# Kernel optimization log

Measured on AMD Instinct MI355X. Metric: run time of the kernel, lower is better.

Reference implementation:

```python
import jax, jax.numpy as jnp
import numpy as np

POOL = 7  # pool_size


def _src_coords(start, size, P):
    """TF1 resize_images bilinear (align_corners=False): src = out_idx * in/out.
    start,size: (R,) int32 crop offset/extent. Returns abs low/high idx and frac, all (R,P)."""
    j = jnp.arange(P, dtype=jnp.float32)  # (P,)
    s = j[None, :] * (size[:, None].astype(jnp.float32) / P)  # (R,P) coords inside crop
    i0 = jnp.floor(s).astype(jnp.int32)
    i1 = jnp.minimum(i0 + 1, size[:, None] - 1)
    frac = s - i0.astype(jnp.float32)
    return start[:, None] + i0, start[:, None] + i1, frac


def roi_pool(img, rois, P):
    # img: (1,H,W,C) float; rois: (1,R,4) as (x,y,w,h) -> cast to int32 like the original
    im = img[0]  # (H,W,C)
    r = rois[0].astype(jnp.int32)  # (R,4)
    x, y, w, h = r[:, 0], r[:, 1], r[:, 2], r[:, 3]
    H, W = im.shape[0], im.shape[1]
    ax0, ax1, fx = _src_coords(x, w, P)  # (R,P)
    ay0, ay1, fy = _src_coords(y, h, P)  # (R,P)
    ax0 = jnp.clip(ax0, 0, W - 1); ax1 = jnp.clip(ax1, 0, W - 1)
    ay0 = jnp.clip(ay0, 0, H - 1); ay1 = jnp.clip(ay1, 0, H - 1)
    # broadcasted corner gathers -> (R,P,P,C)
    v00 = im[ay0[:, :, None], ax0[:, None, :]]
    v01 = im[ay0[:, :, None], ax1[:, None, :]]
    v10 = im[ay1[:, :, None], ax0[:, None, :]]
    v11 = im[ay1[:, :, None], ax1[:, None, :]]
    fx_ = fx[:, None, :, None]  # broadcast over y-dim and channels
    fy_ = fy[:, :, None, None]
    top = v00 * (1.0 - fx_) + v01 * fx_
    bot = v10 * (1.0 - fx_) + v11 * fx_
    out = top * (1.0 - fy_) + bot * fy_  # (R,P,P,C)
    return out[None]  # (1,R,P,P,C)


def setup_inputs() -> dict:
    key = jax.random.key(0)
    k1, k2, k3, k4, k5 = jax.random.split(key, 5)
    H = W = 100
    C = 1024
    R = 512
    img = jax.random.normal(k1, (1, H, W, C), dtype=jnp.float32)
    x = jax.random.randint(k2, (1, R), 0, 50)
    y = jax.random.randint(k3, (1, R), 0, 50)
    w = jax.random.randint(k4, (1, R), 1, 51)
    h = jax.random.randint(k5, (1, R), 1, 51)
    rois = jnp.stack([x, y, w, h], axis=-1).astype(jnp.float32)  # (1,R,4)
    return {"img": img, "rois": rois}


def reference(img, rois):
    return roi_pool(img, rois, POOL)
```

## Files before the change

kernel.cpp:

```cpp
#include <hip/hip_runtime.h>


#define IMG_H 100
#define IMG_W 100
#define IMG_C 1024
#define N_ROI 512
#define POOLP 7

__global__ __launch_bounds__(256) void roi_pool_kernel(
    const float* __restrict__ img,
    const float* __restrict__ rois,
    float* __restrict__ out)
{
    const int p   = blockIdx.x;
    const int roi = p / 49;
    const int pos = p - roi * 49;
    const int py  = pos / 7;
    const int px  = pos - py * 7;

    const float4 rv = *reinterpret_cast<const float4*>(rois + roi * 4);
    const int x = (int)rv.x;
    const int y = (int)rv.y;
    const int w = (int)rv.z;
    const int h = (int)rv.w;

    const float sx  = (float)px * ((float)w / (float)POOLP);
    const int   ix0 = (int)floorf(sx);
    const int   ix1 = min(ix0 + 1, w - 1);
    const float fx  = sx - (float)ix0;
    const int   ax0 = min(max(x + ix0, 0), IMG_W - 1);
    const int   ax1 = min(max(x + ix1, 0), IMG_W - 1);

    const float sy  = (float)py * ((float)h / (float)POOLP);
    const int   iy0 = (int)floorf(sy);
    const int   iy1 = min(iy0 + 1, h - 1);
    const float fy  = sy - (float)iy0;
    const int   ay0 = min(max(y + iy0, 0), IMG_H - 1);
    const int   ay1 = min(max(y + iy1, 0), IMG_H - 1);

    const float gx = 1.0f - fx;
    const float gy = 1.0f - fy;

    const int c = threadIdx.x << 2;

    const float4 v00 = *reinterpret_cast<const float4*>(
        img + ((size_t)ay0 * IMG_W + ax0) * IMG_C + c);
    const float4 v01 = *reinterpret_cast<const float4*>(
        img + ((size_t)ay0 * IMG_W + ax1) * IMG_C + c);
    const float4 v10 = *reinterpret_cast<const float4*>(
        img + ((size_t)ay1 * IMG_W + ax0) * IMG_C + c);
    const float4 v11 = *reinterpret_cast<const float4*>(
        img + ((size_t)ay1 * IMG_W + ax1) * IMG_C + c);

    float4 o;
    o.x = (v00.x * gx + v01.x * fx) * gy + (v10.x * gx + v11.x * fx) * fy;
    o.y = (v00.y * gx + v01.y * fx) * gy + (v10.y * gx + v11.y * fx) * fy;
    o.z = (v00.z * gx + v01.z * fx) * gy + (v10.z * gx + v11.z * fx) * fy;
    o.w = (v00.w * gx + v01.w * fx) * gy + (v10.w * gx + v11.w * fx) * fy;

    *reinterpret_cast<float4*>(out + (size_t)p * IMG_C + c) = o;
}

extern "C" void kernel_launch(void* const* d_in, const int* in_sizes, int n_in,
                              void* d_out, int out_size, void* d_ws, size_t ws_size,
                              hipStream_t stream)
{
    const float* img  = (const float*)d_in[0];
    const float* rois = (const float*)d_in[1];
    float* out = (float*)d_out;

    const int n_blocks = N_ROI * POOLP * POOLP;
    roi_pool_kernel<<<n_blocks, 256, 0, stream>>>(img, rois, out);
}
```

Measured before the change: 162.4 us.

## Use persistent blocks with software-pipelined gathers, XCD-aware block mapping, nontemporal stores

```diff
diff --git a/kernel.cpp b/kernel.cpp
--- a/kernel.cpp
+++ b/kernel.cpp
@@ -6,19 +6,23 @@
 #define IMG_C 1024
 #define N_ROI 512
 #define POOLP 7
+#define NPOS  (N_ROI * POOLP * POOLP)
+#define NBLK  2048
 
-__global__ __launch_bounds__(256) void roi_pool_kernel(
-    const float* __restrict__ img,
-    const float* __restrict__ rois,
-    float* __restrict__ out)
+typedef float f32x4 __attribute__((ext_vector_type(4)));
+
+__device__ __forceinline__ void pos_setup(
+    const float* __restrict__ img, const float* __restrict__ rois,
+    int p, int c,
+    const f32x4*& q00, const f32x4*& q01, const f32x4*& q10, const f32x4*& q11,
+    float& fx, float& fy)
 {
-    const int p   = blockIdx.x;
     const int roi = p / 49;
     const int pos = p - roi * 49;
     const int py  = pos / 7;
     const int px  = pos - py * 7;
 
-    const float4 rv = *reinterpret_cast<const float4*>(rois + roi * 4);
+    const f32x4 rv = *reinterpret_cast<const f32x4*>(rois + roi * 4);
     const int x = (int)rv.x;
     const int y = (int)rv.y;
     const int w = (int)rv.z;
@@ -27,38 +31,74 @@
     const float sx  = (float)px * ((float)w / (float)POOLP);
     const int   ix0 = (int)floorf(sx);
     const int   ix1 = min(ix0 + 1, w - 1);
-    const float fx  = sx - (float)ix0;
-    const int   ax0 = min(max(x + ix0, 0), IMG_W - 1);
-    const int   ax1 = min(max(x + ix1, 0), IMG_W - 1);
+    fx = sx - (float)ix0;
+    const int ax0 = min(max(x + ix0, 0), IMG_W - 1);
+    const int ax1 = min(max(x + ix1, 0), IMG_W - 1);
 
     const float sy  = (float)py * ((float)h / (float)POOLP);
     const int   iy0 = (int)floorf(sy);
     const int   iy1 = min(iy0 + 1, h - 1);
-    const float fy  = sy - (float)iy0;
-    const int   ay0 = min(max(y + iy0, 0), IMG_H - 1);
-    const int   ay1 = min(max(y + iy1, 0), IMG_H - 1);
+    fy = sy - (float)iy0;
+    const int ay0 = min(max(y + iy0, 0), IMG_H - 1);
+    const int ay1 = min(max(y + iy1, 0), IMG_H - 1);
 
+    q00 = reinterpret_cast<const f32x4*>(img + ((size_t)(ay0 * IMG_W + ax0) * IMG_C + c));
+    q01 = reinterpret_cast<const f32x4*>(img + ((size_t)(ay0 * IMG_W + ax1) * IMG_C + c));
+    q10 = reinterpret_cast<const f32x4*>(img + ((size_t)(ay1 * IMG_W + ax0) * IMG_C + c));
+    q11 = reinterpret_cast<const f32x4*>(img + ((size_t)(ay1 * IMG_W + ax1) * IMG_C + c));
+}
+
+__device__ __forceinline__ f32x4 blend(
+    f32x4 v00, f32x4 v01, f32x4 v10, f32x4 v11, float fx, float fy)
+{
     const float gx = 1.0f - fx;
     const float gy = 1.0f - fy;
+    f32x4 top = v00 * gx + v01 * fx;
+    f32x4 bot = v10 * gx + v11 * fx;
+    return top * gy + bot * fy;
+}
+
+__global__ __launch_bounds__(256) void roi_pool_kernel(
+    const float* __restrict__ img,
+    const float* __restrict__ rois,
+    float* __restrict__ out)
+{
+    const int b = blockIdx.x;
+    const int cid = ((b & 7) << 8) | (b >> 3);
+    const int p0  = (int)(((long long)cid       * NPOS) / NBLK);
+    const int p1  = (int)(((long long)(cid + 1) * NPOS) / NBLK);
+    if (p0 >= p1) return;
 
     const int c = threadIdx.x << 2;
 
-    const float4 v00 = *reinterpret_cast<const float4*>(
-        img + ((size_t)ay0 * IMG_W + ax0) * IMG_C + c);
-    const float4 v01 = *reinterpret_cast<const float4*>(
-        img + ((size_t)ay0 * IMG_W + ax1) * IMG_C + c);
-    const float4 v10 = *reinterpret_cast<const float4*>(
-        img + ((size_t)ay1 * IMG_W + ax0) * IMG_C + c);
-    const float4 v11 = *reinterpret_cast<const float4*>(
-        img + ((size_t)ay1 * IMG_W + ax1) * IMG_C + c);
+    const f32x4 *q00, *q01, *q10, *q11;
+    float fx, fy;
+    pos_setup(img, rois, p0, c, q00, q01, q10, q11, fx, fy);
+    f32x4 v00 = *q00;
+    f32x4 v01 = *q01;
+    f32x4 v10 = *q10;
+    f32x4 v11 = *q11;
 
-    float4 o;
-    o.x = (v00.x * gx + v01.x * fx) * gy + (v10.x * gx + v11.x * fx) * fy;
-    o.y = (v00.y * gx + v01.y * fx) * gy + (v10.y * gx + v11.y * fx) * fy;
-    o.z = (v00.z * gx + v01.z * fx) * gy + (v10.z * gx + v11.z * fx) * fy;
-    o.w = (v00.w * gx + v01.w * fx) * gy + (v10.w * gx + v11.w * fx) * fy;
+    for (int p = p0 + 1; p < p1; ++p) {
+        const f32x4 *r00, *r01, *r10, *r11;
+        float nfx, nfy;
+        pos_setup(img, rois, p, c, r00, r01, r10, r11, nfx, nfy);
+        f32x4 w00 = *r00;
+        f32x4 w01 = *r01;
+        f32x4 w10 = *r10;
+        f32x4 w11 = *r11;
 
-    *reinterpret_cast<float4*>(out + (size_t)p * IMG_C + c) = o;
+        const f32x4 o = blend(v00, v01, v10, v11, fx, fy);
+        __builtin_nontemporal_store(
+            o, reinterpret_cast<f32x4*>(out + (size_t)(p - 1) * IMG_C + c));
+
+        v00 = w00; v01 = w01; v10 = w10; v11 = w11;
+        fx = nfx; fy = nfy;
+    }
+
+    const f32x4 o = blend(v00, v01, v10, v11, fx, fy);
+    __builtin_nontemporal_store(
+        o, reinterpret_cast<f32x4*>(out + (size_t)(p1 - 1) * IMG_C + c));
 }
 
 extern "C" void kernel_launch(void* const* d_in, const int* in_sizes, int n_in,
@@ -69,6 +109,5 @@
     const float* rois = (const float*)d_in[1];
     float* out = (float*)d_out;
 
-    const int n_blocks = N_ROI * POOLP * POOLP;
-    roi_pool_kernel<<<n_blocks, 256, 0, stream>>>(img, rois, out);
+    roi_pool_kernel<<<NBLK, 256, 0, stream>>>(img, rois, out);
 }
```

After: 169.2 us. 1.04x slower.

## Persistent grid with XCD-aware ROI partitioning and nontemporal output stores

Applied to the files above, without the earlier changes.

```diff
diff --git a/kernel.cpp b/kernel.cpp
--- a/kernel.cpp
+++ b/kernel.cpp
@@ -6,59 +6,83 @@
 #define IMG_C 1024
 #define N_ROI 512
 #define POOLP 7
+#define NPOS  (N_ROI * POOLP * POOLP)
+#define NBLK  4096
+#define ROI_PER_XCD   (N_ROI / 8)
+#define UNITS_PER_XCD (ROI_PER_XCD * 49)
+#define BLK_PER_XCD   (NBLK / 8)
 
-__global__ __launch_bounds__(256) void roi_pool_kernel(
+typedef float f32x4 __attribute__((ext_vector_type(4)));
+
+__global__ __launch_bounds__(128) void roi_pool_kernel(
     const float* __restrict__ img,
     const float* __restrict__ rois,
     float* __restrict__ out)
 {
-    const int p   = blockIdx.x;
-    const int roi = p / 49;
-    const int pos = p - roi * 49;
-    const int py  = pos / 7;
-    const int px  = pos - py * 7;
+    const int b    = blockIdx.x;
+    const int xcd  = b & 7;
+    const int l    = b >> 3;
+    const int base = xcd * UNITS_PER_XCD;
 
-    const float4 rv = *reinterpret_cast<const float4*>(rois + roi * 4);
-    const int x = (int)rv.x;
-    const int y = (int)rv.y;
-    const int w = (int)rv.z;
-    const int h = (int)rv.w;
+    const int c0 = threadIdx.x << 2;
+    const int c1 = c0 + 512;
 
-    const float sx  = (float)px * ((float)w / (float)POOLP);
-    const int   ix0 = (int)floorf(sx);
-    const int   ix1 = min(ix0 + 1, w - 1);
-    const float fx  = sx - (float)ix0;
-    const int   ax0 = min(max(x + ix0, 0), IMG_W - 1);
-    const int   ax1 = min(max(x + ix1, 0), IMG_W - 1);
+    for (int u = l; u < UNITS_PER_XCD; u += BLK_PER_XCD) {
+        const int p   = base + u;
+        const int roi = p / 49;
+        const int pos = p - roi * 49;
+        const int py  = pos / 7;
+        const int px  = pos - py * 7;
 
-    const float sy  = (float)py * ((float)h / (float)POOLP);
-    const int   iy0 = (int)floorf(sy);
-    const int   iy1 = min(iy0 + 1, h - 1);
-    const float fy  = sy - (float)iy0;
-    const int   ay0 = min(max(y + iy0, 0), IMG_H - 1);
-    const int   ay1 = min(max(y + iy1, 0), IMG_H - 1);
+        const f32x4 rv = *reinterpret_cast<const f32x4*>(rois + roi * 4);
+        const int x = (int)rv.x;
+        const int y = (int)rv.y;
+        const int w = (int)rv.z;
+        const int h = (int)rv.w;
 
-    const float gx = 1.0f - fx;
-    const float gy = 1.0f - fy;
+        const float sx  = (float)px * ((float)w / (float)POOLP);
+        const int   ix0 = (int)floorf(sx);
+        const int   ix1 = min(ix0 + 1, w - 1);
+        const float fx  = sx - (float)ix0;
+        const int ax0 = min(max(x + ix0, 0), IMG_W - 1);
+        const int ax1 = min(max(x + ix1, 0), IMG_W - 1);
 
-    const int c = threadIdx.x << 2;
+        const float sy  = (float)py * ((float)h / (float)POOLP);
+        const int   iy0 = (int)floorf(sy);
+        const int   iy1 = min(iy0 + 1, h - 1);
+        const float fy  = sy - (float)iy0;
+        const int ay0 = min(max(y + iy0, 0), IMG_H - 1);
+        const int ay1 = min(max(y + iy1, 0), IMG_H - 1);
 
-    const float4 v00 = *reinterpret_cast<const float4*>(
-        img + ((size_t)ay0 * IMG_W + ax0) * IMG_C + c);
-    const float4 v01 = *reinterpret_cast<const float4*>(
-        img + ((size_t)ay0 * IMG_W + ax1) * IMG_C + c);
-    const float4 v10 = *reinterpret_cast<const float4*>(
-        img + ((size_t)ay1 * IMG_W + ax0) * IMG_C + c);
-    const float4 v11 = *reinterpret_cast<const float4*>(
-        img + ((size_t)ay1 * IMG_W + ax1) * IMG_C + c);
+        const float* b00 = img + (size_t)(ay0 * IMG_W + ax0) * IMG_C;
+        const float* b01 = img + (size_t)(ay0 * IMG_W + ax1) * IMG_C;
+        const float* b10 = img + (size_t)(ay1 * IMG_W + ax0) * IMG_C;
+        const float* b11 = img + (size_t)(ay1 * IMG_W + ax1) * IMG_C;
 
-    float4 o;
-    o.x = (v00.x * gx + v01.x * fx) * gy + (v10.x * gx + v11.x * fx) * fy;
-    o.y = (v00.y * gx + v01.y * fx) * gy + (v10.y * gx + v11.y * fx) * fy;
-    o.z = (v00.z * gx + v01.z * fx) * gy + (v10.z * gx + v11.z * fx) * fy;
-    o.w = (v00.w * gx + v01.w * fx) * gy + (v10.w * gx + v11.w * fx) * fy;
+        const f32x4 a00 = *reinterpret_cast<const f32x4*>(b00 + c0);
+        const f32x4 a01 = *reinterpret_cast<const f32x4*>(b01 + c0);
+        const f32x4 a10 = *reinterpret_cast<const f32x4*>(b10 + c0);
+        const f32x4 a11 = *reinterpret_cast<const f32x4*>(b11 + c0);
+        const f32x4 d00 = *reinterpret_cast<const f32x4*>(b00 + c1);
+        const f32x4 d01 = *reinterpret_cast<const f32x4*>(b01 + c1);
+        const f32x4 d10 = *reinterpret_cast<const f32x4*>(b10 + c1);
+        const f32x4 d11 = *reinterpret_cast<const f32x4*>(b11 + c1);
 
-    *reinterpret_cast<float4*>(out + (size_t)p * IMG_C + c) = o;
+        const float gx = 1.0f - fx;
+        const float gy = 1.0f - fy;
+
+        f32x4 topA = a00 * gx + a01 * fx;
+        f32x4 botA = a10 * gx + a11 * fx;
+        f32x4 oA   = topA * gy + botA * fy;
+
+        f32x4 topD = d00 * gx + d01 * fx;
+        f32x4 botD = d10 * gx + d11 * fx;
+        f32x4 oD   = topD * gy + botD * fy;
+
+        float* ob = out + (size_t)p * IMG_C;
+        __builtin_nontemporal_store(oA, reinterpret_cast<f32x4*>(ob + c0));
+        __builtin_nontemporal_store(oD, reinterpret_cast<f32x4*>(ob + c1));
+    }
 }
 
 extern "C" void kernel_launch(void* const* d_in, const int* in_sizes, int n_in,
@@ -69,6 +93,5 @@
     const float* rois = (const float*)d_in[1];
     float* out = (float*)d_out;
 
-    const int n_blocks = N_ROI * POOLP * POOLP;
-    roi_pool_kernel<<<n_blocks, 256, 0, stream>>>(img, rois, out);
+    roi_pool_kernel<<<NBLK, 128, 0, stream>>>(img, rois, out);
 }
```

After: 160.9 us. Within noise of the previous version (-1.0%).
